# Performance work log

Hardware: AMD Instinct MI355X
Metric: run time of the kernel (lower is better)

## Reference

```python
import jax, jax.numpy as jnp
import numpy as np

B, S, E, H = 2, 2048, 2048, 16
D = E // H  # head_dim = 128


def setup_inputs() -> dict:
    key = jax.random.key(0)
    ks = jax.random.split(key, 7)
    x = jax.random.normal(ks[0], (B, S, E), dtype=jnp.float32)
    cos = jax.random.uniform(ks[1], (S, D), dtype=jnp.float32)
    sin = jax.random.uniform(ks[2], (S, D), dtype=jnp.float32)
    scale = 1.0 / np.sqrt(E)
    Wq = jax.random.normal(ks[3], (E, E), dtype=jnp.float32) * scale
    Wk = jax.random.normal(ks[4], (E, E), dtype=jnp.float32) * scale
    Wv = jax.random.normal(ks[5], (E, E), dtype=jnp.float32) * scale
    Wo = jax.random.normal(ks[6], (E, E), dtype=jnp.float32) * scale
    return {"x": x, "cos": cos, "sin": sin, "Wq": Wq, "Wk": Wk, "Wv": Wv, "Wo": Wo}


def _apply_rope(t, cos, sin):
    # t: [B, S, H, D]; cos/sin: [S, D]. NeoX rotate-half.
    half = t.shape[-1] // 2
    rotate = jnp.concatenate([-t[..., half:], t[..., :half]], axis=-1)
    return t * cos[None, :, None, :] + rotate * sin[None, :, None, :]


def reference(x, cos, sin, Wq, Wk, Wv, Wo):
    b, s, e = x.shape
    q = (x @ Wq.T).reshape(b, s, H, D)
    k = (x @ Wk.T).reshape(b, s, H, D)
    v = (x @ Wv.T).reshape(b, s, H, D)
    q = _apply_rope(q, cos, sin).transpose(0, 2, 1, 3)  # [B,H,S,D]
    k = _apply_rope(k, cos, sin).transpose(0, 2, 1, 3)
    v = v.transpose(0, 2, 1, 3)
    scale = 1.0 / jnp.sqrt(jnp.asarray(D, dtype=x.dtype))
    scores = jnp.einsum("bhqd,bhkd->bhqk", q, k) * scale
    causal = jnp.tril(jnp.ones((s, s), dtype=bool))
    scores = jnp.where(causal[None, None], scores, jnp.asarray(-1e30, dtype=scores.dtype))
    attn = jax.nn.softmax(scores, axis=-1)
    out = jnp.einsum("bhqk,bhkd->bhqd", attn, v)  # [B,H,S,D]
    out = out.transpose(0, 2, 1, 3).reshape(b, s, e)
    return out @ Wo.T
```

## Files before the change

kernel.cpp:

```cpp
#include <hip/hip_runtime.h>
#include <stdint.h>

typedef unsigned short u16;
typedef __attribute__((ext_vector_type(8))) short short8;
typedef __attribute__((ext_vector_type(4))) float f32x4;
typedef __attribute__((ext_vector_type(16))) float f32x16;

#define B_ 2
#define S_ 2048
#define E_ 2048
#define H_ 16
#define D_ 128
#define M_ 4096

__device__ __forceinline__ u16 f2bf(float f) {
  unsigned u = __float_as_uint(f);
  u = u + 0x7FFFu + ((u >> 16) & 1u);
  return (u16)(u >> 16);
}
__device__ __forceinline__ float bf2f(u16 h) {
  return __uint_as_float(((unsigned)h) << 16);
}

#define GLD16(gp, lp) __builtin_amdgcn_global_load_lds(                      \
    (__attribute__((address_space(1))) void*)(gp),                           \
    (__attribute__((address_space(3))) void*)(lp), 16, 0, 0)

__global__ void cast_bf16(const float4* __restrict__ src, ushort4* __restrict__ dst, int n4) {
  int i = blockIdx.x * 256 + threadIdx.x;
  if (i < n4) {
    float4 v = src[i];
    ushort4 o;
    o.x = f2bf(v.x); o.y = f2bf(v.y); o.z = f2bf(v.z); o.w = f2bf(v.w);
    dst[i] = o;
  }
}

__global__ void cast4_bf16(const float4* __restrict__ w0, const float4* __restrict__ w1,
                           const float4* __restrict__ w2, const float4* __restrict__ w3,
                           ushort4* __restrict__ o0, ushort4* __restrict__ o1,
                           ushort4* __restrict__ o2, ushort4* __restrict__ o3, int n4) {
  const int i = blockIdx.x * 256 + threadIdx.x;
  if (i >= n4) return;
  const float4* s; ushort4* d;
  switch (blockIdx.y) {
    case 0: s = w0; d = o0; break;
    case 1: s = w1; d = o1; break;
    case 2: s = w2; d = o2; break;
    default: s = w3; d = o3; break;
  }
  float4 v = s[i];
  ushort4 o;
  o.x = f2bf(v.x); o.y = f2bf(v.y); o.z = f2bf(v.z); o.w = f2bf(v.w);
  d[i] = o;
}

template <int MODE>
__launch_bounds__(512, 1)
__global__ void gemm256(const u16* __restrict__ A, const u16* __restrict__ Bw,
                        void* __restrict__ Cp, int M, int N, int K, int bxpx) {
  __shared__ alignas(16) u16 LA[3][128 * 64];
  __shared__ alignas(16) u16 LB[3][256 * 64];
  const int tid = threadIdx.x, wave = tid >> 6, lane = tid & 63;
  const int xcd = blockIdx.x & 7;
  const int j = blockIdx.x >> 3;
  const int bx = xcd * bxpx + (j % bxpx);
  const int by = j / bxpx;
  const int m0 = by * 128, n0 = bx * 256;
  const int wm = (wave >> 2) * 64, wn = (wave & 3) * 64;
  const int lrow = lane & 15, lq = lane >> 4;

  auto stage0 = [&](int buf, int kt) {
    const int k0 = kt * 64;
#pragma unroll
    for (int i = 0; i < 2; ++i) {
      const int c = i * 512 + tid;
      const int row = c >> 3, k = c & 7;
      GLD16(A + (size_t)(m0 + row) * K + k0 + ((k ^ (row & 7)) * 8),
            &LA[buf][i * 4096 + wave * 512]);
    }
    {
      const int c = tid;
      const int row = c >> 3, k = c & 7;
      GLD16(Bw + (size_t)(n0 + row) * K + k0 + ((k ^ (row & 7)) * 8),
            &LB[buf][wave * 512]);
    }
  };
  auto stage1 = [&](int buf, int kt) {
    const int k0 = kt * 64;
#pragma unroll
    for (int i = 1; i < 4; ++i) {
      const int c = i * 512 + tid;
      const int row = c >> 3, k = c & 7;
      GLD16(Bw + (size_t)(n0 + row) * K + k0 + ((k ^ (row & 7)) * 8),
            &LB[buf][i * 4096 + wave * 512]);
    }
  };

  f32x4 acc[4][4] = {};
  const int NT = K >> 6;
  stage0(0, 0); stage1(0, 0);
  stage0(1, 1); stage1(1, 1);
  asm volatile("s_waitcnt vmcnt(6)" ::: "memory");
  __builtin_amdgcn_sched_barrier(0);
  __builtin_amdgcn_s_barrier();

  for (int t = 0; t < NT; ++t) {
    const int cur = t % 3;
    const int sb = (t + 2) % 3;
    const bool dostage = (t + 2) < NT;

    short8 a0[4], b0[4];
#pragma unroll
    for (int m = 0; m < 4; ++m) {
      const int row = wm + m * 16 + lrow;
      a0[m] = *(const short8*)&LA[cur][row * 64 + ((lq ^ (row & 7)) * 8)];
    }
#pragma unroll
    for (int n = 0; n < 4; ++n) {
      const int row = wn + n * 16 + lrow;
      b0[n] = *(const short8*)&LB[cur][row * 64 + ((lq ^ (row & 7)) * 8)];
    }
    if (dostage) stage0(sb, t + 2);
    __builtin_amdgcn_sched_barrier(0);
    __builtin_amdgcn_s_barrier();
    __builtin_amdgcn_sched_barrier(0);
    __builtin_amdgcn_s_setprio(1);
#pragma unroll
    for (int m = 0; m < 4; ++m)
#pragma unroll
      for (int n = 0; n < 4; ++n)
        acc[m][n] = __builtin_amdgcn_mfma_f32_16x16x32_bf16(a0[m], b0[n], acc[m][n], 0, 0, 0);
    __builtin_amdgcn_s_setprio(0);
    __builtin_amdgcn_sched_barrier(0);
    __builtin_amdgcn_s_barrier();

    short8 a1[4], b1[4];
#pragma unroll
    for (int m = 0; m < 4; ++m) {
      const int row = wm + m * 16 + lrow;
      a1[m] = *(const short8*)&LA[cur][row * 64 + (((4 + lq) ^ (row & 7)) * 8)];
    }
#pragma unroll
    for (int n = 0; n < 4; ++n) {
      const int row = wn + n * 16 + lrow;
      b1[n] = *(const short8*)&LB[cur][row * 64 + (((4 + lq) ^ (row & 7)) * 8)];
    }
    if (dostage) stage1(sb, t + 2);
    if (t < NT - 2)      { asm volatile("s_waitcnt vmcnt(6)" ::: "memory"); }
    else if (t == NT - 2){ asm volatile("s_waitcnt vmcnt(0)" ::: "memory"); }
    __builtin_amdgcn_sched_barrier(0);
    __builtin_amdgcn_s_barrier();
    __builtin_amdgcn_sched_barrier(0);
    __builtin_amdgcn_s_setprio(1);
#pragma unroll
    for (int m = 0; m < 4; ++m)
#pragma unroll
      for (int n = 0; n < 4; ++n)
        acc[m][n] = __builtin_amdgcn_mfma_f32_16x16x32_bf16(a1[m], b1[n], acc[m][n], 0, 0, 0);
    __builtin_amdgcn_s_setprio(0);
    __builtin_amdgcn_sched_barrier(0);
    __builtin_amdgcn_s_barrier();
  }

  const int rbase = lq * 4;
#pragma unroll
  for (int m = 0; m < 4; ++m)
#pragma unroll
    for (int n = 0; n < 4; ++n)
#pragma unroll
      for (int r = 0; r < 4; ++r) {
        const int mm = m0 + wm + m * 16 + rbase + r;
        const int nn = n0 + wn + n * 16 + lrow;
        const float v = acc[m][n][r];
        if (MODE == 0) {
          const size_t NXc = (size_t)B_ * S_ * E_;
          const int bb = mm >> 11, s = mm & (S_ - 1);
          const int tz = nn >> 11, nc = nn & 2047;
          const int h = nc >> 7, d = nc & (D_ - 1);
          ((u16*)Cp)[(size_t)tz * NXc + (((size_t)bb * H_ + h) * S_ + s) * D_ + d] = f2bf(v);
        } else {
          ((float*)Cp)[(size_t)mm * N + nn] = v;
        }
      }
}

__global__ void rope2_k(u16* __restrict__ Qb, u16* __restrict__ Kb,
                        const float* __restrict__ cosT, const float* __restrict__ sinT) {
  const int y = blockIdx.y;
  u16* T = y ? Kb : Qb;
  const float sc = y ? 1.f : 0.12751744154f;
  const int idx = blockIdx.x * 256 + threadIdx.x;
  const int row = idx >> 3;
  const int d0 = (idx & 7) * 8;
  const int s = row & (S_ - 1);
  const size_t base = (size_t)row * D_;
  short8 lo = *(const short8*)&T[base + d0];
  short8 hv = *(const short8*)&T[base + d0 + 64];
  float c1v[8], s1v[8], c2v[8], s2v[8];
  *(float4*)&c1v[0] = *(const float4*)&cosT[s * D_ + d0];
  *(float4*)&c1v[4] = *(const float4*)&cosT[s * D_ + d0 + 4];
  *(float4*)&s1v[0] = *(const float4*)&sinT[s * D_ + d0];
  *(float4*)&s1v[4] = *(const float4*)&sinT[s * D_ + d0 + 4];
  *(float4*)&c2v[0] = *(const float4*)&cosT[s * D_ + d0 + 64];
  *(float4*)&c2v[4] = *(const float4*)&cosT[s * D_ + d0 + 68];
  *(float4*)&s2v[0] = *(const float4*)&sinT[s * D_ + d0 + 64];
  *(float4*)&s2v[4] = *(const float4*)&sinT[s * D_ + d0 + 68];
  short8 olo, ohi;
#pragma unroll
  for (int j = 0; j < 8; ++j) {
    const float x1 = bf2f((u16)lo[j]), x2 = bf2f((u16)hv[j]);
    olo[j] = (short)f2bf((x1 * c1v[j] - x2 * s1v[j]) * sc);
    ohi[j] = (short)f2bf((x2 * c2v[j] + x1 * s2v[j]) * sc);
  }
  *(short8*)&T[base + d0] = olo;
  *(short8*)&T[base + d0 + 64] = ohi;
}

__global__ void transpose64(const u16* __restrict__ V, u16* __restrict__ VT) {
  __shared__ alignas(16) u16 t[64][72];
  const int bh = blockIdx.z, st = blockIdx.y * 64, dt = blockIdx.x * 64;
  const u16* Vp = V + (size_t)bh * S_ * D_;
  u16* Tp = VT + (size_t)bh * D_ * S_;
  const int tid = threadIdx.x;
#pragma unroll
  for (int p = 0; p < 2; ++p) {
    const int idx = p * 256 + tid;
    const int r = idx >> 3, c8 = (idx & 7) * 8;
    *(short8*)&t[r][c8] = *(const short8*)&Vp[(size_t)(st + r) * D_ + dt + c8];
  }
  __syncthreads();
#pragma unroll
  for (int p = 0; p < 2; ++p) {
    const int idx = p * 256 + tid;
    const int dr = idx >> 3, s8 = (idx & 7) * 8;
    short8 v;
#pragma unroll
    for (int j = 0; j < 8; ++j) v[j] = t[s8 + j][dr];
    *(short8*)&Tp[(size_t)(dt + dr) * S_ + st + s8] = v;
  }
}

__launch_bounds__(512, 2)
__global__ void attn_fwd(const u16* __restrict__ Q, const u16* __restrict__ Kt,
                         const u16* __restrict__ VT, u16* __restrict__ Out) {
  __shared__ alignas(16) u16 SB[2][2][16384];
  __shared__ float MLB[4][64][2];
  const int tid = threadIdx.x, wave = tid >> 6, lane = tid & 63;
  const int hw = blockIdx.x;
  const int lid = (hw & 7) * 32 + (hw >> 3);
  const int p = lid & 7, bh = lid >> 3;
  const int bb = bh >> 4, h = bh & 15;
  const u16* Qh = Q + (size_t)bh * S_ * D_;
  const u16* Kh = Kt + (size_t)bh * S_ * D_;
  const u16* Vh = VT + (size_t)bh * D_ * S_;
  const int grp = wave >> 2, w4 = wave & 3;
  const int l31 = lane & 31, hi = lane >> 5;

  auto stage = [&](int buf, int kv0) {
#pragma unroll
    for (int pp = 0; pp < 4; ++pp) {
      const int g = pp * 4 + w4;
      const int c = g * 64 + lane;
      const int srow = c >> 4, dch = c & 15;
      GLD16(Kh + (size_t)(kv0 + srow) * D_ + ((dch ^ (srow & 7)) * 8), &SB[grp][buf][g * 512]);
      const int drow = c >> 3, sch = c & 7;
      GLD16(Vh + (size_t)drow * S_ + kv0 + ((sch ^ (drow & 7)) * 8), &SB[grp][buf][8192 + g * 512]);
    }
  };

  float* obuf = (float*)&SB[1][0][0];

  const int qts[2] = {15 - p, p};
#pragma unroll 1
  for (int seg = 0; seg < 2; ++seg) {
    const int t = qts[seg];
    const int iters = t + 1;
    const int q0 = t * 128 + w4 * 32;
    const int qg = q0 + l31;

    short8 qf[8];
#pragma unroll
    for (int m = 0; m < 8; ++m)
      qf[m] = *(const short8*)&Qh[(size_t)qg * D_ + m * 16 + hi * 8];

    f32x16 od[4] = {};
    float mr = 0.f, lsum = 0.f;

    stage(0, grp * 64);
    int cur = 0;

    for (int i = 0; i < iters; ++i) {
      __syncthreads();
      if (i + 1 < iters) stage(cur ^ 1, (2 * (i + 1) + grp) * 64);
      const int kv0 = (2 * i + grp) * 64;
      const u16* Kc = &SB[grp][cur][0];
      const u16* Vc = &SB[grp][cur][8192];

      f32x16 s0 = {}, s1 = {};
      __builtin_amdgcn_s_setprio(1);
#pragma unroll
      for (int m = 0; m < 8; ++m) {
        const int col = m * 16 + hi * 8;
        const int sw = (l31 & 7) << 3;
        short8 k0 = *(const short8*)&Kc[l31 * 128 + (col ^ sw)];
        short8 k1 = *(const short8*)&Kc[(32 + l31) * 128 + (col ^ sw)];
        s0 = __builtin_amdgcn_mfma_f32_32x32x16_bf16(k0, qf[m], s0, 0, 0, 0);
        s1 = __builtin_amdgcn_mfma_f32_32x32x16_bf16(k1, qf[m], s1, 0, 0, 0);
      }
      __builtin_amdgcn_s_setprio(0);

      if (kv0 + 63 > q0) {
#pragma unroll
        for (int r = 0; r < 16; ++r) {
          const int k0g = kv0 + (r & 3) + 8 * (r >> 2) + 4 * hi;
          if (k0g > qg)      s0[r] = -1e30f;
          if (k0g + 32 > qg) s1[r] = -1e30f;
        }
      }

      float mloc = s0[0];
#pragma unroll
      for (int r = 1; r < 16; ++r) mloc = fmaxf(mloc, s0[r]);
#pragma unroll
      for (int r = 0; r < 16; ++r) mloc = fmaxf(mloc, s1[r]);
      const float mx = fmaxf(mloc, __shfl_xor(mloc, 32));
      const bool need = !__all(mx <= mr + 8.f);
      float corr = 1.f;
      if (need) {
        const float mnew = fmaxf(mr, mx);
        corr = exp2f(mr - mnew);
        mr = mnew;
      }
      float sloc = 0.f;
#pragma unroll
      for (int r = 0; r < 16; ++r) { s0[r] = exp2f(s0[r] - mr); sloc += s0[r]; }
#pragma unroll
      for (int r = 0; r < 16; ++r) { s1[r] = exp2f(s1[r] - mr); sloc += s1[r]; }
      const float rsum = sloc + __shfl_xor(sloc, 32);
      lsum = lsum * corr + rsum;
      if (need) {
#pragma unroll
        for (int dt = 0; dt < 4; ++dt)
#pragma unroll
          for (int r = 0; r < 16; ++r) od[dt][r] *= corr;
      }

      unsigned W0[4][2], W1[4][2];
#pragma unroll
      for (int c = 0; c < 4; ++c)
#pragma unroll
        for (int pr = 0; pr < 2; ++pr) {
          asm("v_cvt_pk_bf16_f32 %0, %1, %2"
              : "=v"(W0[c][pr]) : "v"(s0[4 * c + 2 * pr]), "v"(s0[4 * c + 2 * pr + 1]));
          asm("v_cvt_pk_bf16_f32 %0, %1, %2"
              : "=v"(W1[c][pr]) : "v"(s1[4 * c + 2 * pr]), "v"(s1[4 * c + 2 * pr + 1]));
        }

      __builtin_amdgcn_s_setprio(1);
#pragma unroll
      for (int kk = 0; kk < 4; ++kk) {
        const int cown = 2 * (kk & 1) + hi, csend = 2 * (kk & 1) + 1 - hi;
        unsigned o0, o1, sd0, sd1;
        if (kk < 2) { o0 = W0[cown][0]; o1 = W0[cown][1]; sd0 = W0[csend][0]; sd1 = W0[csend][1]; }
        else        { o0 = W1[cown][0]; o1 = W1[cown][1]; sd0 = W1[csend][0]; sd1 = W1[csend][1]; }
        const unsigned r0 = (unsigned)__shfl_xor((int)sd0, 32);
        const unsigned r1 = (unsigned)__shfl_xor((int)sd1, 32);
        uint4 bw;
        if (hi == 0) bw = make_uint4(o0, o1, r0, r1);
        else         bw = make_uint4(r0, r1, o0, o1);
        const short8 pf = *(const short8*)&bw;
        const int slot = 2 * kk + hi;
#pragma unroll
        for (int dt = 0; dt < 4; ++dt) {
          const int row = dt * 32 + l31;
          const short8 vf = *(const short8*)&Vc[row * 64 + ((slot ^ (row & 7)) * 8)];
          od[dt] = __builtin_amdgcn_mfma_f32_32x32x16_bf16(vf, pf, od[dt], 0, 0, 0);
        }
      }
      __builtin_amdgcn_s_setprio(0);
      cur ^= 1;
    }

    __syncthreads();
    if (grp == 1) {
      MLB[w4][lane][0] = mr;
      MLB[w4][lane][1] = lsum;
#pragma unroll
      for (int dt = 0; dt < 4; ++dt)
#pragma unroll
        for (int r = 0; r < 16; ++r)
          obuf[(dt * 16 + r) * 256 + w4 * 64 + lane] = od[dt][r];
    }
    __syncthreads();
    if (grp == 0) {
      const float mB = MLB[w4][lane][0];
      const float lB = MLB[w4][lane][1];
      const float m = fmaxf(mr, mB);
      const float aA = exp2f(mr - m), aB = exp2f(mB - m);
      lsum = lsum * aA + lB * aB;
#pragma unroll
      for (int dt = 0; dt < 4; ++dt)
#pragma unroll
        for (int r = 0; r < 16; ++r)
          od[dt][r] = od[dt][r] * aA + obuf[(dt * 16 + r) * 256 + w4 * 64 + lane] * aB;

      const float inv = 1.f / lsum;
      const size_t obase = ((size_t)bb * S_ + qg) * E_ + h * D_;
#pragma unroll
      for (int dt = 0; dt < 4; ++dt)
#pragma unroll
        for (int g = 0; g < 4; ++g) {
          ushort4 w;
          w.x = f2bf(od[dt][4 * g + 0] * inv);
          w.y = f2bf(od[dt][4 * g + 1] * inv);
          w.z = f2bf(od[dt][4 * g + 2] * inv);
          w.w = f2bf(od[dt][4 * g + 3] * inv);
          *(ushort4*)&Out[obase + dt * 32 + 8 * g + 4 * hi] = w;
        }
    }
    __syncthreads();
  }
}

extern "C" void kernel_launch(void* const* d_in, const int* in_sizes, int n_in,
                              void* d_out, int out_size, void* d_ws, size_t ws_size,
                              hipStream_t stream) {
  const float* x    = (const float*)d_in[0];
  const float* cosT = (const float*)d_in[1];
  const float* sinT = (const float*)d_in[2];
  const float* Wq   = (const float*)d_in[3];
  const float* Wk   = (const float*)d_in[4];
  const float* Wv   = (const float*)d_in[5];
  const float* Wo   = (const float*)d_in[6];
  float* out = (float*)d_out;

  const size_t NX = (size_t)B_ * S_ * E_;
  const size_t NW = (size_t)E_ * E_;
  u16* ws  = (u16*)d_ws;
  u16* xb  = ws;
  u16* Wqb = xb + NX;
  u16* Wkb = Wqb + NW;
  u16* Wvb = Wkb + NW;
  u16* Wob = Wvb + NW;
  u16* Qb  = Wob + NW;
  u16* Kb  = Qb + NX;
  u16* Vb  = Kb + NX;
  u16* VTb = Vb + NX;
  u16* Ab  = VTb + NX;

  cast_bf16<<<(int)(NX / 4 / 256), 256, 0, stream>>>((const float4*)x, (ushort4*)xb, (int)(NX / 4));
  cast4_bf16<<<dim3((int)(NW / 4 / 256), 4), 256, 0, stream>>>(
      (const float4*)Wq, (const float4*)Wk, (const float4*)Wv, (const float4*)Wo,
      (ushort4*)Wqb, (ushort4*)Wkb, (ushort4*)Wvb, (ushort4*)Wob, (int)(NW / 4));

  gemm256<0><<<dim3(768), 512, 0, stream>>>(xb, Wqb, Qb, M_, 3 * E_, E_, 3);

  rope2_k<<<dim3((B_ * H_ * S_ * 8) / 256, 2), 256, 0, stream>>>(Qb, Kb, cosT, sinT);

  transpose64<<<dim3(D_ / 64, S_ / 64, B_ * H_), 256, 0, stream>>>(Vb, VTb);

  attn_fwd<<<dim3(256), 512, 0, stream>>>(Qb, Kb, VTb, Ab);

  gemm256<1><<<dim3(256), 512, 0, stream>>>(Ab, Wob, out, M_, E_, E_, 1);
}
```

Measured before the change: 271.9 us.

## Fuse RoPE and V transpose into QKV GEMM epilogue via LDS staging

The QKV projection GEMM epilogue now stages the bf16 tile in shared memory, then applies RoPE (with the Q scale) for Q/K tiles or writes V directly in transposed layout. This removes the separate rope and transpose kernels and their global round trips. It also removes two of the four barriers per K iteration in the GEMM main loop, relying on the triple buffer and lgkmcnt waits for safety. The risks are a slower epilogue from LDS staging and scattered cos/sin loads, and possible races from the removed barriers.

```diff
diff --git a/kernel.cpp b/kernel.cpp
--- a/kernel.cpp
+++ b/kernel.cpp
@@ -58,9 +58,11 @@
 template <int MODE>
 __launch_bounds__(512, 1)
 __global__ void gemm256(const u16* __restrict__ A, const u16* __restrict__ Bw,
-                        void* __restrict__ Cp, int M, int N, int K, int bxpx) {
-  __shared__ alignas(16) u16 LA[3][128 * 64];
-  __shared__ alignas(16) u16 LB[3][256 * 64];
+                        void* __restrict__ Cp, int M, int N, int K, int bxpx,
+                        const float* __restrict__ cosT, const float* __restrict__ sinT) {
+  __shared__ alignas(16) u16 SMEM[73728];
+  u16* const LA = SMEM;
+  u16* const LB = SMEM + 24576;
   const int tid = threadIdx.x, wave = tid >> 6, lane = tid & 63;
   const int xcd = blockIdx.x & 7;
   const int j = blockIdx.x >> 3;
@@ -77,13 +79,13 @@
       const int c = i * 512 + tid;
       const int row = c >> 3, k = c & 7;
       GLD16(A + (size_t)(m0 + row) * K + k0 + ((k ^ (row & 7)) * 8),
-            &LA[buf][i * 4096 + wave * 512]);
+            LA + buf * 8192 + i * 4096 + wave * 512);
     }
     {
       const int c = tid;
       const int row = c >> 3, k = c & 7;
       GLD16(Bw + (size_t)(n0 + row) * K + k0 + ((k ^ (row & 7)) * 8),
-            &LB[buf][wave * 512]);
+            LB + buf * 16384 + wave * 512);
     }
   };
   auto stage1 = [&](int buf, int kt) {
@@ -93,7 +95,7 @@
       const int c = i * 512 + tid;
       const int row = c >> 3, k = c & 7;
       GLD16(Bw + (size_t)(n0 + row) * K + k0 + ((k ^ (row & 7)) * 8),
-            &LB[buf][i * 4096 + wave * 512]);
+            LB + buf * 16384 + i * 4096 + wave * 512);
     }
   };
 
@@ -101,7 +103,7 @@
   const int NT = K >> 6;
   stage0(0, 0); stage1(0, 0);
   stage0(1, 1); stage1(1, 1);
-  asm volatile("s_waitcnt vmcnt(6)" ::: "memory");
+  asm volatile("s_waitcnt vmcnt(6) lgkmcnt(0)" ::: "memory");
   __builtin_amdgcn_sched_barrier(0);
   __builtin_amdgcn_s_barrier();
 
@@ -114,12 +116,12 @@
 #pragma unroll
     for (int m = 0; m < 4; ++m) {
       const int row = wm + m * 16 + lrow;
-      a0[m] = *(const short8*)&LA[cur][row * 64 + ((lq ^ (row & 7)) * 8)];
+      a0[m] = *(const short8*)&LA[cur * 8192 + row * 64 + ((lq ^ (row & 7)) * 8)];
     }
 #pragma unroll
     for (int n = 0; n < 4; ++n) {
       const int row = wn + n * 16 + lrow;
-      b0[n] = *(const short8*)&LB[cur][row * 64 + ((lq ^ (row & 7)) * 8)];
+      b0[n] = *(const short8*)&LB[cur * 16384 + row * 64 + ((lq ^ (row & 7)) * 8)];
     }
     if (dostage) stage0(sb, t + 2);
     __builtin_amdgcn_sched_barrier(0);
@@ -132,23 +134,21 @@
       for (int n = 0; n < 4; ++n)
         acc[m][n] = __builtin_amdgcn_mfma_f32_16x16x32_bf16(a0[m], b0[n], acc[m][n], 0, 0, 0);
     __builtin_amdgcn_s_setprio(0);
-    __builtin_amdgcn_sched_barrier(0);
-    __builtin_amdgcn_s_barrier();
 
     short8 a1[4], b1[4];
 #pragma unroll
     for (int m = 0; m < 4; ++m) {
       const int row = wm + m * 16 + lrow;
-      a1[m] = *(const short8*)&LA[cur][row * 64 + (((4 + lq) ^ (row & 7)) * 8)];
+      a1[m] = *(const short8*)&LA[cur * 8192 + row * 64 + (((4 + lq) ^ (row & 7)) * 8)];
     }
 #pragma unroll
     for (int n = 0; n < 4; ++n) {
       const int row = wn + n * 16 + lrow;
-      b1[n] = *(const short8*)&LB[cur][row * 64 + (((4 + lq) ^ (row & 7)) * 8)];
+      b1[n] = *(const short8*)&LB[cur * 16384 + row * 64 + (((4 + lq) ^ (row & 7)) * 8)];
     }
     if (dostage) stage1(sb, t + 2);
-    if (t < NT - 2)      { asm volatile("s_waitcnt vmcnt(6)" ::: "memory"); }
-    else if (t == NT - 2){ asm volatile("s_waitcnt vmcnt(0)" ::: "memory"); }
+    if (t < NT - 2) { asm volatile("s_waitcnt vmcnt(6) lgkmcnt(0)" ::: "memory"); }
+    else            { asm volatile("s_waitcnt vmcnt(0) lgkmcnt(0)" ::: "memory"); }
     __builtin_amdgcn_sched_barrier(0);
     __builtin_amdgcn_s_barrier();
     __builtin_amdgcn_sched_barrier(0);
@@ -159,85 +159,82 @@
       for (int n = 0; n < 4; ++n)
         acc[m][n] = __builtin_amdgcn_mfma_f32_16x16x32_bf16(a1[m], b1[n], acc[m][n], 0, 0, 0);
     __builtin_amdgcn_s_setprio(0);
-    __builtin_amdgcn_sched_barrier(0);
-    __builtin_amdgcn_s_barrier();
   }
 
   const int rbase = lq * 4;
+  if (MODE == 1) {
+#pragma unroll
+    for (int m = 0; m < 4; ++m)
+#pragma unroll
+      for (int n = 0; n < 4; ++n)
+#pragma unroll
+        for (int r = 0; r < 4; ++r) {
+          const int mm = m0 + wm + m * 16 + rbase + r;
+          const int nn = n0 + wn + n * 16 + lrow;
+          ((float*)Cp)[(size_t)mm * N + nn] = acc[m][n][r];
+        }
+    return;
+  }
+
+  u16* ct = SMEM;
 #pragma unroll
   for (int m = 0; m < 4; ++m)
 #pragma unroll
     for (int n = 0; n < 4; ++n)
 #pragma unroll
-      for (int r = 0; r < 4; ++r) {
-        const int mm = m0 + wm + m * 16 + rbase + r;
-        const int nn = n0 + wn + n * 16 + lrow;
-        const float v = acc[m][n][r];
-        if (MODE == 0) {
-          const size_t NXc = (size_t)B_ * S_ * E_;
-          const int bb = mm >> 11, s = mm & (S_ - 1);
-          const int tz = nn >> 11, nc = nn & 2047;
-          const int h = nc >> 7, d = nc & (D_ - 1);
-          ((u16*)Cp)[(size_t)tz * NXc + (((size_t)bb * H_ + h) * S_ + s) * D_ + d] = f2bf(v);
-        } else {
-          ((float*)Cp)[(size_t)mm * N + nn] = v;
-        }
-      }
-}
-
-__global__ void rope2_k(u16* __restrict__ Qb, u16* __restrict__ Kb,
-                        const float* __restrict__ cosT, const float* __restrict__ sinT) {
-  const int y = blockIdx.y;
-  u16* T = y ? Kb : Qb;
-  const float sc = y ? 1.f : 0.12751744154f;
-  const int idx = blockIdx.x * 256 + threadIdx.x;
-  const int row = idx >> 3;
-  const int d0 = (idx & 7) * 8;
-  const int s = row & (S_ - 1);
-  const size_t base = (size_t)row * D_;
-  short8 lo = *(const short8*)&T[base + d0];
-  short8 hv = *(const short8*)&T[base + d0 + 64];
-  float c1v[8], s1v[8], c2v[8], s2v[8];
-  *(float4*)&c1v[0] = *(const float4*)&cosT[s * D_ + d0];
-  *(float4*)&c1v[4] = *(const float4*)&cosT[s * D_ + d0 + 4];
-  *(float4*)&s1v[0] = *(const float4*)&sinT[s * D_ + d0];
-  *(float4*)&s1v[4] = *(const float4*)&sinT[s * D_ + d0 + 4];
-  *(float4*)&c2v[0] = *(const float4*)&cosT[s * D_ + d0 + 64];
-  *(float4*)&c2v[4] = *(const float4*)&cosT[s * D_ + d0 + 68];
-  *(float4*)&s2v[0] = *(const float4*)&sinT[s * D_ + d0 + 64];
-  *(float4*)&s2v[4] = *(const float4*)&sinT[s * D_ + d0 + 68];
-  short8 olo, ohi;
-#pragma unroll
-  for (int j = 0; j < 8; ++j) {
-    const float x1 = bf2f((u16)lo[j]), x2 = bf2f((u16)hv[j]);
-    olo[j] = (short)f2bf((x1 * c1v[j] - x2 * s1v[j]) * sc);
-    ohi[j] = (short)f2bf((x2 * c2v[j] + x1 * s2v[j]) * sc);
-  }
-  *(short8*)&T[base + d0] = olo;
-  *(short8*)&T[base + d0 + 64] = ohi;
-}
-
-__global__ void transpose64(const u16* __restrict__ V, u16* __restrict__ VT) {
-  __shared__ alignas(16) u16 t[64][72];
-  const int bh = blockIdx.z, st = blockIdx.y * 64, dt = blockIdx.x * 64;
-  const u16* Vp = V + (size_t)bh * S_ * D_;
-  u16* Tp = VT + (size_t)bh * D_ * S_;
-  const int tid = threadIdx.x;
-#pragma unroll
-  for (int p = 0; p < 2; ++p) {
-    const int idx = p * 256 + tid;
-    const int r = idx >> 3, c8 = (idx & 7) * 8;
-    *(short8*)&t[r][c8] = *(const short8*)&Vp[(size_t)(st + r) * D_ + dt + c8];
-  }
+      for (int r = 0; r < 4; ++r)
+        ct[(wm + m * 16 + rbase + r) * 272 + wn + n * 16 + lrow] = f2bf(acc[m][n][r]);
   __syncthreads();
-#pragma unroll
-  for (int p = 0; p < 2; ++p) {
-    const int idx = p * 256 + tid;
-    const int dr = idx >> 3, s8 = (idx & 7) * 8;
-    short8 v;
-#pragma unroll
-    for (int j = 0; j < 8; ++j) v[j] = t[s8 + j][dr];
-    *(short8*)&Tp[(size_t)(dt + dr) * S_ + st + s8] = v;
+
+  const int tz = n0 >> 11;
+  const int bb = m0 >> 11, s0 = m0 & (S_ - 1);
+  const int h0 = (n0 >> 7) & 15;
+  const size_t NXc = (size_t)B_ * S_ * E_;
+  u16* dst = (u16*)Cp + (size_t)tz * NXc;
+
+  if (tz < 2) {
+    const float sc = (tz == 0) ? 0.12751744154f : 1.f;
+#pragma unroll
+    for (int i = 0; i < 8; ++i) {
+      const int idx = i * 512 + tid;
+      const int row = idx >> 5, c8 = (idx & 31) * 8;
+      const int head = c8 >> 7, hd = c8 & 127;
+      const int s = s0 + row;
+      short8 self = *(const short8*)&ct[row * 272 + c8];
+      short8 part = *(const short8*)&ct[row * 272 + (c8 ^ 64)];
+      float4 cv0 = *(const float4*)&cosT[s * D_ + hd];
+      float4 cv1 = *(const float4*)&cosT[s * D_ + hd + 4];
+      float4 sv0 = *(const float4*)&sinT[s * D_ + hd];
+      float4 sv1 = *(const float4*)&sinT[s * D_ + hd + 4];
+      float cv[8] = {cv0.x, cv0.y, cv0.z, cv0.w, cv1.x, cv1.y, cv1.z, cv1.w};
+      float sv[8] = {sv0.x, sv0.y, sv0.z, sv0.w, sv1.x, sv1.y, sv1.z, sv1.w};
+      short8 o;
+      if (hd < 64) {
+#pragma unroll
+        for (int jj = 0; jj < 8; ++jj) {
+          const float x1 = bf2f((u16)self[jj]), x2 = bf2f((u16)part[jj]);
+          o[jj] = (short)f2bf((x1 * cv[jj] - x2 * sv[jj]) * sc);
+        }
+      } else {
+#pragma unroll
+        for (int jj = 0; jj < 8; ++jj) {
+          const float x2 = bf2f((u16)self[jj]), x1 = bf2f((u16)part[jj]);
+          o[jj] = (short)f2bf((x2 * cv[jj] + x1 * sv[jj]) * sc);
+        }
+      }
+      *(short8*)&dst[(((size_t)bb * H_ + h0 + head) * S_ + s) * D_ + hd] = o;
+    }
+  } else {
+#pragma unroll
+    for (int i = 0; i < 8; ++i) {
+      const int task = i * 512 + tid;
+      const int dcol = task & 255, sch = task >> 8;
+      short8 v;
+#pragma unroll
+      for (int jj = 0; jj < 8; ++jj) v[jj] = ct[(sch * 8 + jj) * 272 + dcol];
+      const int h = h0 + (dcol >> 7), hd = dcol & 127;
+      *(short8*)&dst[(((size_t)bb * H_ + h) * D_ + hd) * S_ + s0 + sch * 8] = v;
+    }
   }
 }
 
@@ -445,8 +442,7 @@
   u16* Wob = Wvb + NW;
   u16* Qb  = Wob + NW;
   u16* Kb  = Qb + NX;
-  u16* Vb  = Kb + NX;
-  u16* VTb = Vb + NX;
+  u16* VTb = Kb + NX;
   u16* Ab  = VTb + NX;
 
   cast_bf16<<<(int)(NX / 4 / 256), 256, 0, stream>>>((const float4*)x, (ushort4*)xb, (int)(NX / 4));
@@ -454,13 +450,9 @@
       (const float4*)Wq, (const float4*)Wk, (const float4*)Wv, (const float4*)Wo,
       (ushort4*)Wqb, (ushort4*)Wkb, (ushort4*)Wvb, (ushort4*)Wob, (int)(NW / 4));
 
-  gemm256<0><<<dim3(768), 512, 0, stream>>>(xb, Wqb, Qb, M_, 3 * E_, E_, 3);
-
-  rope2_k<<<dim3((B_ * H_ * S_ * 8) / 256, 2), 256, 0, stream>>>(Qb, Kb, cosT, sinT);
-
-  transpose64<<<dim3(D_ / 64, S_ / 64, B_ * H_), 256, 0, stream>>>(Vb, VTb);
+  gemm256<0><<<dim3(768), 512, 0, stream>>>(xb, Wqb, Qb, M_, 3 * E_, E_, 3, cosT, sinT);
 
   attn_fwd<<<dim3(256), 512, 0, stream>>>(Qb, Kb, VTb, Ab);
 
-  gemm256<1><<<dim3(256), 512, 0, stream>>>(Ab, Wob, out, M_, E_, E_, 1);
-}
+  gemm256<1><<<dim3(256), 512, 0, stream>>>(Ab, Wob, out, M_, E_, E_, 1, nullptr, nullptr);
+}
```

Result: faster. 249.0 us (-8.4%).
